# Kernel tuning notes

Measured on AMD Instinct MI355X. Metric: run time of the kernel, lower is better.

The kernel has to match this reference:

```python
import jax, jax.numpy as jnp
import numpy as np

GROUPS = 8
EPS = 1e-5
PERM_IN = {'x': (0, 2, 4, 1, 3), 'y': (0, 2, 3, 1, 4), 'seq': (0, 3, 4, 1, 2)}
PERM_OUT = {'x': (0, 3, 1, 4, 2), 'y': (0, 3, 1, 2, 4), 'seq': (0, 3, 4, 1, 2)}


def bn_train(x, gamma, beta, axis=1):
    """Training-mode batch norm: normalize over all axes except `axis`."""
    axes = tuple(i for i in range(x.ndim) if i != axis)
    mean = x.mean(axes, keepdims=True)
    var = x.var(axes, keepdims=True)
    shp = [1] * x.ndim
    shp[axis] = x.shape[axis]
    return (x - mean) * jax.lax.rsqrt(var + EPS) * gamma.reshape(shp) + beta.reshape(shp)


def axial_attn(x, qkv_w, gq, bq, gs, bs, go, bo, direction):
    # x: (N, C, seq, H, W)
    x = jnp.transpose(x, PERM_IN[direction])
    N, seq, W, C, H = x.shape
    B = N * seq * W
    xf = x.reshape(B, C, H)
    # 1x1 conv1d qkv projection + BN over channels
    qkv = jnp.einsum('oc,bch->boh', qkv_w, xf)            # (B, 2C, H)
    qkv = bn_train(qkv, gq, bq, axis=1)
    gp = C // GROUPS                                       # group_planes
    qkv = qkv.reshape(B, GROUPS, 2 * gp, H)
    q = qkv[:, :, : gp // 2]
    k = qkv[:, :, gp // 2: gp]
    v = qkv[:, :, gp:]
    qk = jnp.einsum('bgci,bgcj->bgij', q, k)               # (B, g, H, H)
    qk = bn_train(qk, gs, bs, axis=1)
    sim = jax.nn.softmax(qk, axis=3)
    sv = jnp.einsum('bgij,bgcj->bgci', sim, v)             # (B, g, gp, H)
    sv = bn_train(sv.reshape(B, C, H), go, bo, axis=1)
    out = sv.reshape(N, seq, W, C, H)
    return jnp.transpose(out, PERM_OUT[direction])


def setup_inputs() -> dict:
    key = jax.random.key(0)
    ks = jax.random.split(key, 4)
    N, C_in, seq, H, W = 2, 128, 16, 56, 56
    width = 64
    x = jax.random.normal(ks[0], (N, C_in, seq, H, W), jnp.float32)
    cd_w = jax.random.normal(ks[1], (width, C_in), jnp.float32) * (1.0 / np.sqrt(C_in))
    qkv_w = jax.random.normal(ks[2], (3, 2 * width, width), jnp.float32) * (1.0 / np.sqrt(width))
    cu_w = jax.random.normal(ks[3], (2 * width, width), jnp.float32) * (1.0 / np.sqrt(width))
    return {
        'x': x,
        'cd_w': cd_w,
        'bn1_g': jnp.ones((width,), jnp.float32),
        'bn1_b': jnp.zeros((width,), jnp.float32),
        'qkv_w': qkv_w,
        'bnq_g': jnp.ones((3, 2 * width), jnp.float32),
        'bnq_b': jnp.zeros((3, 2 * width), jnp.float32),
        'bns_g': jnp.ones((3, GROUPS), jnp.float32),
        'bns_b': jnp.zeros((3, GROUPS), jnp.float32),
        'bno_g': jnp.ones((3, width), jnp.float32),
        'bno_b': jnp.zeros((3, width), jnp.float32),
        'cu_w': cu_w,
        'bn2_g': jnp.ones((2 * width,), jnp.float32),
        'bn2_b': jnp.zeros((2 * width,), jnp.float32),
    }


def reference(x, cd_w, bn1_g, bn1_b, qkv_w, bnq_g, bnq_b, bns_g, bns_b,
              bno_g, bno_b, cu_w, bn2_g, bn2_b):
    identity = x
    out = jnp.einsum('oc,ncshw->noshw', cd_w, x)           # conv_down (1x1)
    out = jax.nn.relu(bn_train(out, bn1_g, bn1_b, axis=1))
    for i, d in enumerate(('x', 'y', 'seq')):              # height, width, seq axial passes
        out = axial_attn(out, qkv_w[i], bnq_g[i], bnq_b[i], bns_g[i], bns_b[i],
                         bno_g[i], bno_b[i], d)
    out = jax.nn.relu(out)
    out = jnp.einsum('oc,ncshw->noshw', cu_w, out)         # conv_up (1x1)
    out = bn_train(out, bn2_g, bn2_b, axis=1)
    return jax.nn.relu(out + identity)
```

## Files before the change

### kernel.cpp

```cpp
#include <hip/hip_runtime.h>

constexpr int SP = 16*56*56;
constexpr int P  = 2*SP;
constexpr float EPSV = 1e-5f;

constexpr size_t SZ_A   = (size_t)2*64*SP;
constexpr size_t OFF_A  = 0;
constexpr size_t OFF_C  = SZ_A;
constexpr size_t OFF_ST = OFF_C + SZ_A;
constexpr size_t OFF_P1 = 0;
constexpr size_t OFF_P2 = 65536;

__global__ void __launch_bounds__(256) kern_down(
    const float* __restrict__ x, const float* __restrict__ w,
    float* __restrict__ A, float* __restrict__ st)
{
  __shared__ float xs[128*64];
  __shared__ float wt[64*129];
  __shared__ float ssum[64], ssq[64];
  const int t = threadIdx.x;
  if (t < 64) { ssum[t] = 0.f; ssq[t] = 0.f; }
  const int p0 = blockIdx.x * 64;
  const int n = p0 / SP, rem = p0 % SP;
  const float* xb = x + (size_t)n*128*SP + rem;
  for (int e4 = t; e4 < 128*16; e4 += 256) {
    int c = e4 >> 4, p4 = (e4 & 15)*4;
    float4 v = *reinterpret_cast<const float4*>(xb + (size_t)c*SP + p4);
    *reinterpret_cast<float4*>(&xs[c*64 + p4]) = v;
  }
  for (int e4 = t; e4 < 64*32; e4 += 256) {
    int o = e4 >> 5, c4 = (e4 & 31)*4;
    float4 v = *reinterpret_cast<const float4*>(w + o*128 + c4);
    *reinterpret_cast<float4*>(&wt[o*129 + c4]) = v;
  }
  __syncthreads();
  const int og = t & 15, pg = t >> 4;
  float acc[4][4] = {};
  for (int c = 0; c < 128; ++c) {
    float xv[4], wv[4];
    #pragma unroll
    for (int j = 0; j < 4; ++j) xv[j] = xs[c*64 + pg*4 + j];
    #pragma unroll
    for (int i = 0; i < 4; ++i) wv[i] = wt[(og + 16*i)*129 + c];
    #pragma unroll
    for (int i = 0; i < 4; ++i) {
      #pragma unroll
      for (int j = 0; j < 4; ++j) acc[i][j] = fmaf(wv[i], xv[j], acc[i][j]);
    }
  }
  float* Ab = A + (size_t)n*64*SP + rem;
  #pragma unroll
  for (int i = 0; i < 4; ++i) {
    const int o = og + 16*i;
    float s1 = 0.f, s2 = 0.f;
    #pragma unroll
    for (int j = 0; j < 4; ++j) { float v = acc[i][j]; s1 += v; s2 += v*v; }
    float4 v4 = make_float4(acc[i][0], acc[i][1], acc[i][2], acc[i][3]);
    *reinterpret_cast<float4*>(Ab + (size_t)o*SP + pg*4) = v4;
    atomicAdd(&ssum[o], s1);
    atomicAdd(&ssq[o], s2);
  }
  __syncthreads();
  if (t < 64) { atomicAdd(&st[t], ssum[t]); atomicAdd(&st[64+t], ssq[t]); }
}

__global__ void __launch_bounds__(256) kern_tr(
    const float* __restrict__ A, float* __restrict__ At)
{
  __shared__ float tile[56*57];
  const size_t base = (size_t)blockIdx.x*3136;
  for (int e4 = threadIdx.x; e4 < 784; e4 += 256) {
    int e = e4*4, h = e/56, w = e%56;
    float4 v = *reinterpret_cast<const float4*>(A + base + e);
    tile[w*57+h] = v.x; tile[(w+1)*57+h] = v.y;
    tile[(w+2)*57+h] = v.z; tile[(w+3)*57+h] = v.w;
  }
  __syncthreads();
  for (int e4 = threadIdx.x; e4 < 784; e4 += 256) {
    int e = e4*4, w = e/56, h = e%56;
    float4 v = make_float4(tile[w*57+h], tile[w*57+h+1], tile[w*57+h+2], tile[w*57+h+3]);
    *reinterpret_cast<float4*>(At + base + e) = v;
  }
}

__global__ void __launch_bounds__(256) kern_up(
    const float* __restrict__ A, const float* __restrict__ w,
    float* __restrict__ U, float* __restrict__ st)
{
  __shared__ float xs[64*64];
  __shared__ float wt[128*65];
  __shared__ float ssum[128], ssq[128];
  const int t = threadIdx.x;
  if (t < 128) { ssum[t]=0.f; ssq[t]=0.f; }
  const int p0 = blockIdx.x*64;
  const int n = p0/SP, rem = p0%SP;
  const float* Ab = A + (size_t)n*64*SP + rem;
  for (int e4 = t; e4 < 64*16; e4 += 256) {
    int c = e4 >> 4, p4 = (e4 & 15)*4;
    float4 v = *reinterpret_cast<const float4*>(Ab + (size_t)c*SP + p4);
    v.x = fmaxf(v.x, 0.f); v.y = fmaxf(v.y, 0.f); v.z = fmaxf(v.z, 0.f); v.w = fmaxf(v.w, 0.f);
    *reinterpret_cast<float4*>(&xs[c*64 + p4]) = v;
  }
  for (int e4 = t; e4 < 128*16; e4 += 256) {
    int o = e4 >> 4, c4 = (e4 & 15)*4;
    float4 v = *reinterpret_cast<const float4*>(w + o*64 + c4);
    *reinterpret_cast<float4*>(&wt[o*65 + c4]) = v;
  }
  __syncthreads();
  const int og = t & 31, pg = t >> 5;
  float acc[4][8] = {};
  for (int c = 0; c < 64; ++c) {
    float xv[8];
    #pragma unroll
    for (int j = 0; j < 8; ++j) xv[j] = xs[c*64 + pg*8 + j];
    #pragma unroll
    for (int i = 0; i < 4; ++i) {
      float wv = wt[(og + 32*i)*65 + c];
      #pragma unroll
      for (int j = 0; j < 8; ++j) acc[i][j] = fmaf(wv, xv[j], acc[i][j]);
    }
  }
  float* Ub = U + (size_t)n*128*SP + rem;
  #pragma unroll
  for (int i = 0; i < 4; ++i) {
    const int o = og + 32*i;
    float s1=0.f, s2=0.f;
    #pragma unroll
    for (int j = 0; j < 8; ++j) { float v = acc[i][j]; s1 += v; s2 += v*v; }
    float4 a = make_float4(acc[i][0],acc[i][1],acc[i][2],acc[i][3]);
    float4 b = make_float4(acc[i][4],acc[i][5],acc[i][6],acc[i][7]);
    *reinterpret_cast<float4*>(Ub + (size_t)o*SP + pg*8)     = a;
    *reinterpret_cast<float4*>(Ub + (size_t)o*SP + pg*8 + 4) = b;
    atomicAdd(&ssum[o], s1); atomicAdd(&ssq[o], s2);
  }
  __syncthreads();
  if (t < 128) { atomicAdd(&st[t], ssum[t]); atomicAdd(&st[128+t], ssq[t]); }
}

template<bool FIRST>
__global__ void __launch_bounds__(256) kern_qkv(
    const float* __restrict__ src, const float* __restrict__ w,
    const float* __restrict__ sc1, const float* __restrict__ sh1,
    float* __restrict__ Bq, float* __restrict__ st)
{
  constexpr int H = 56;
  __shared__ float xs[64*H];
  __shared__ float wt[128*65];
  __shared__ float ssum[128], ssq[128];
  const int t = threadIdx.x;
  if (t < 128) { ssum[t]=0.f; ssq[t]=0.f; }
  const int b = blockIdx.x;
  const int n = b/896, r = b%896, s = r/56, q = r%56;
  const size_t base = (size_t)n*64*SP + s*3136 + q*56;
  for (int e4 = t; e4 < 64*14; e4 += 256) {
    int c = e4/14, j4 = (e4%14)*4;
    float4 v = *reinterpret_cast<const float4*>(src + base + (size_t)c*SP + j4);
    if (FIRST) {
      float sc = sc1[c], sh = sh1[c];
      v.x = fmaxf(fmaf(v.x, sc, sh), 0.f); v.y = fmaxf(fmaf(v.y, sc, sh), 0.f);
      v.z = fmaxf(fmaf(v.z, sc, sh), 0.f); v.w = fmaxf(fmaf(v.w, sc, sh), 0.f);
    }
    xs[c*H + j4]   = v.x; xs[c*H + j4+1] = v.y;
    xs[c*H + j4+2] = v.z; xs[c*H + j4+3] = v.w;
  }
  for (int e4 = t; e4 < 128*16; e4 += 256) {
    int o = e4 >> 4, c4 = (e4 & 15)*4;
    float4 v = *reinterpret_cast<const float4*>(w + o*64 + c4);
    *reinterpret_cast<float4*>(&wt[o*65 + c4]) = v;
  }
  __syncthreads();
  const int og = t & 31, hg = t >> 5;
  float acc[4][7] = {};
  for (int c = 0; c < 64; ++c) {
    float xv[7];
    #pragma unroll
    for (int j = 0; j < 7; ++j) xv[j] = xs[c*H + hg*7 + j];
    #pragma unroll
    for (int i = 0; i < 4; ++i) {
      float wv = wt[(og + 32*i)*65 + c];
      #pragma unroll
      for (int j = 0; j < 7; ++j) acc[i][j] = fmaf(wv, xv[j], acc[i][j]);
    }
  }
  float* ob = Bq + (size_t)b*128*H;
  #pragma unroll
  for (int i = 0; i < 4; ++i) {
    const int o = og + 32*i;
    float s1=0.f, s2=0.f;
    #pragma unroll
    for (int j = 0; j < 7; ++j) {
      float v = acc[i][j];
      ob[o*H + hg*7 + j] = v;
      s1 += v; s2 += v*v;
    }
    atomicAdd(&ssum[o], s1); atomicAdd(&ssq[o], s2);
  }
  __syncthreads();
  if (t < 128) { atomicAdd(&st[t], ssum[t]); atomicAdd(&st[128+t], ssq[t]); }
}

__global__ void __launch_bounds__(256) kern_qkv2(
    const float* __restrict__ A, const float* __restrict__ w,
    float* __restrict__ Bq, float* __restrict__ st)
{
  __shared__ float xs[64*64];
  __shared__ float wt[128*65];
  __shared__ float ssum[128], ssq[128];
  const int t = threadIdx.x;
  if (t < 128) { ssum[t]=0.f; ssq[t]=0.f; }
  const int b = blockIdx.x;
  const int n = b/784, r = b%784, y = r/14, w4 = (r%14)*4;
  const float* Ab = A + (size_t)n*64*SP + y*56 + w4;
  for (int e = t; e < 1024; e += 256) {
    int c = e >> 4, s = e & 15;
    float4 v = *reinterpret_cast<const float4*>(Ab + (size_t)c*SP + s*3136);
    xs[c*64 + s]      = v.x;
    xs[c*64 + 16 + s] = v.y;
    xs[c*64 + 32 + s] = v.z;
    xs[c*64 + 48 + s] = v.w;
  }
  for (int e4 = t; e4 < 128*16; e4 += 256) {
    int o = e4 >> 4, c4 = (e4 & 15)*4;
    float4 v = *reinterpret_cast<const float4*>(w + o*64 + c4);
    *reinterpret_cast<float4*>(&wt[o*65 + c4]) = v;
  }
  __syncthreads();
  const int og = t & 31, cg = t >> 5;
  float acc[4][8] = {};
  for (int c = 0; c < 64; ++c) {
    float xv[8];
    #pragma unroll
    for (int j = 0; j < 8; ++j) xv[j] = xs[c*64 + cg*8 + j];
    #pragma unroll
    for (int i = 0; i < 4; ++i) {
      float wv = wt[(og + 32*i)*65 + c];
      #pragma unroll
      for (int j = 0; j < 8; ++j) acc[i][j] = fmaf(wv, xv[j], acc[i][j]);
    }
  }
  const size_t b0 = (size_t)n*3136 + (size_t)y*56 + w4;
  #pragma unroll
  for (int i = 0; i < 4; ++i) {
    const int o = og + 32*i;
    float s1=0.f, s2=0.f;
    #pragma unroll
    for (int j = 0; j < 8; ++j) {
      int col = cg*8 + j, wl = col >> 4, s = col & 15;
      float v = acc[i][j];
      Bq[(b0 + wl)*2048 + o*16 + s] = v;
      s1 += v; s2 += v*v;
    }
    atomicAdd(&ssum[o], s1); atomicAdd(&ssq[o], s2);
  }
  __syncthreads();
  if (t < 128) { atomicAdd(&st[t], ssum[t]); atomicAdd(&st[128+t], ssq[t]); }
}

__global__ void __launch_bounds__(256) kern_redfin(
    const float* __restrict__ part, const float* __restrict__ g,
    const float* __restrict__ b, float* __restrict__ scsh,
    int nb, int nch, float invc)
{
  const int ch = blockIdx.x;
  const int t = threadIdx.x;
  float s1 = 0.f, s2 = 0.f;
  for (int i = t; i < nb; i += 256) {
    s1 += part[(size_t)i*2*nch + ch];
    s2 += part[(size_t)i*2*nch + nch + ch];
  }
  #pragma unroll
  for (int off = 32; off >= 1; off >>= 1) { s1 += __shfl_xor(s1, off); s2 += __shfl_xor(s2, off); }
  __shared__ float r1[4], r2[4];
  if ((t & 63) == 0) { r1[t>>6] = s1; r2[t>>6] = s2; }
  __syncthreads();
  if (t == 0) {
    float S1 = r1[0]+r1[1]+r1[2]+r1[3], S2 = r2[0]+r2[1]+r2[2]+r2[3];
    float mean = S1*invc, var = S2*invc - mean*mean;
    float sc = g[ch]*rsqrtf(var + EPSV);
    scsh[ch] = sc;
    scsh[nch + ch] = b[ch] - mean*sc;
  }
}

template<int H>
__global__ void __launch_bounds__(256) kern_pass1(
    const float* __restrict__ Bq, const float* __restrict__ qsc,
    const float* __restrict__ qsh, float* __restrict__ part)
{
  constexpr int PW = (H==16) ? 4 : 1;
  const int t = threadIdx.x;
  const int wave = t >> 6, lane = t & 63;
  const int sub = (PW==1) ? 0 : (lane >> 4);
  const int i = (PW==1) ? lane : (lane & 15);
  __shared__ float kls[4][4*H*PW];
  __shared__ float bs[16];
  if (t < 16) bs[t] = 0.f;
  float* klw = kls[wave];
  const int pair0 = (blockIdx.x*4 + wave)*PW;
  for (int e = lane; e < 4*H*PW; e += 64) {
    int sp = e / (4*H), r = e % (4*H);
    int c = r / H, j = r % H;
    int pr = pair0 + sp, bb = pr >> 3, g = pr & 7;
    int o = g*16 + 4 + c;
    klw[e] = fmaf(Bq[((size_t)bb*128 + o)*H + j], qsc[o], qsh[o]);
  }
  __syncthreads();
  const int pr = pair0 + sub, bb = pr >> 3, g = pr & 7;
  const float* kp = klw + sub*4*H;
  const bool act = (i < H);
  float q[4];
  #pragma unroll
  for (int c = 0; c < 4; ++c) {
    int o = g*16 + c;
    q[c] = act ? fmaf(Bq[((size_t)bb*128 + o)*H + i], qsc[o], qsh[o]) : 0.f;
  }
  float s1 = 0.f, s2 = 0.f;
  #pragma unroll
  for (int j = 0; j < H; ++j) {
    float s = q[0]*kp[j] + q[1]*kp[H+j] + q[2]*kp[2*H+j] + q[3]*kp[3*H+j];
    s1 += s; s2 += s*s;
  }
  #pragma unroll
  for (int off = (PW==1?32:8); off >= 1; off >>= 1) {
    s1 += __shfl_xor(s1, off);
    s2 += __shfl_xor(s2, off);
  }
  if ((lane & (PW==1?63:15)) == 0) { atomicAdd(&bs[g], s1); atomicAdd(&bs[8+g], s2); }
  __syncthreads();
  if (t < 16) part[(size_t)blockIdx.x*16 + t] = bs[t];
}

template<int H>
__global__ void __launch_bounds__(256) kern_attn(
    const float* __restrict__ Bq, const float* __restrict__ qsc,
    const float* __restrict__ qsh, const float* __restrict__ ssc,
    float* __restrict__ C, float* __restrict__ part)
{
  constexpr int PW = (H==16) ? 4 : 1;
  const int t = threadIdx.x;
  const int wave = t >> 6, lane = t & 63;
  const int sub = (PW==1) ? 0 : (lane >> 4);
  const int i = (PW==1) ? lane : (lane & 15);
  __shared__ float kv[4][12*H*PW];
  __shared__ float bsum[64], bsq[64];
  if (t < 64) { bsum[t] = 0.f; bsq[t] = 0.f; }
  float* kvw = kv[wave];
  const int pair0 = (blockIdx.x*4 + wave)*PW;
  for (int e = lane; e < 12*H*PW; e += 64) {
    int sp = e / (12*H), r = e % (12*H);
    int c = r / H, j = r % H;
    int pr = pair0 + sp, bb = pr >> 3, g = pr & 7;
    int o = g*16 + 4 + c;
    kvw[e] = fmaf(Bq[((size_t)bb*128 + o)*H + j], qsc[o], qsh[o]);
  }
  __syncthreads();
  const int pr = pair0 + sub, bb = pr >> 3, g = pr & 7;
  const float* kp = kvw + sub*12*H;
  const bool act = (i < H);
  float q[4];
  #pragma unroll
  for (int c = 0; c < 4; ++c) {
    int o = g*16 + c;
    q[c] = act ? fmaf(Bq[((size_t)bb*128 + o)*H + i], qsc[o], qsh[o]) : 0.f;
  }
  const float As = ssc[g];
  float m = -3.4e38f;
  for (int j = 0; j < H; ++j) {
    float s = As * (q[0]*kp[j] + q[1]*kp[H+j] + q[2]*kp[2*H+j] + q[3]*kp[3*H+j]);
    m = fmaxf(m, s);
  }
  float den = 0.f;
  float acc[8] = {};
  for (int j = 0; j < H; ++j) {
    float s = As * (q[0]*kp[j] + q[1]*kp[H+j] + q[2]*kp[2*H+j] + q[3]*kp[3*H+j]);
    float e = __expf(s - m);
    den += e;
    #pragma unroll
    for (int c = 0; c < 8; ++c) acc[c] = fmaf(e, kp[(4+c)*H + j], acc[c]);
  }
  const float inv = 1.f/den;
  #pragma unroll
  for (int c = 0; c < 8; ++c) {
    float vv = act ? acc[c]*inv : 0.f;
    if (act) C[((size_t)bb*64 + g*8 + c)*H + i] = vv;
    float s1 = vv, s2 = vv*vv;
    #pragma unroll
    for (int off = (PW==1?32:8); off >= 1; off >>= 1) {
      s1 += __shfl_xor(s1, off);
      s2 += __shfl_xor(s2, off);
    }
    if ((lane & (PW==1?63:15)) == 0) { atomicAdd(&bsum[g*8+c], s1); atomicAdd(&bsq[g*8+c], s2); }
  }
  __syncthreads();
  if (t < 64) {
    part[(size_t)blockIdx.x*128 + t]      = bsum[t];
    part[(size_t)blockIdx.x*128 + 64 + t] = bsq[t];
  }
}

__global__ void __launch_bounds__(256) kern_scat0(
    const float* __restrict__ C, const float* __restrict__ osc,
    const float* __restrict__ osh, float* __restrict__ A)
{
  __shared__ float tile[56*57];
  const int bid = blockIdx.x;
  const int c = bid & 63, s = (bid >> 6) & 15, n = bid >> 10;
  const float sc = osc[c], sh = osh[c];
  const size_t cb = ((size_t)(n*16+s)*56)*3584 + c*56;
  for (int e = threadIdx.x; e < 3136; e += 256) {
    int w = e/56, h = e%56;
    tile[w*57+h] = C[cb + (size_t)w*3584 + h];
  }
  __syncthreads();
  const size_t ab = ((size_t)(n*64+c)*16+s)*3136;
  for (int e = threadIdx.x; e < 3136; e += 256) {
    int h = e/56, w = e%56;
    A[ab + e] = fmaf(tile[w*57+h], sc, sh);
  }
}

__global__ void __launch_bounds__(256) kern_scat1(
    const float* __restrict__ C, const float* __restrict__ osc,
    const float* __restrict__ osh, float* __restrict__ A)
{
  const int e = blockIdx.x*256 + threadIdx.x;
  if (e >= 1792*64*56) return;
  const int w = e % 56, c = (e/56) & 63, b = e / (56*64);
  const int n = b/896, r = b%896, s = r/56, y = r%56;
  A[((size_t)(n*64+c)*16+s)*3136 + y*56 + w] = fmaf(C[e], osc[c], osh[c]);
}

__global__ void __launch_bounds__(256) kern_scat2(
    const float* __restrict__ C, const float* __restrict__ osc,
    const float* __restrict__ osh, float* __restrict__ A)
{
  __shared__ float tile[56*17];
  const int bid = blockIdx.x;
  const int y = bid % 56, c = (bid/56) & 63, n = bid / 3584;
  const float sc = osc[c], sh = osh[c];
  const size_t cb = ((size_t)(n*56+y)*56)*1024 + c*16;
  for (int e = threadIdx.x; e < 896; e += 256) {
    int w = e >> 4, s = e & 15;
    tile[w*17+s] = C[cb + (size_t)w*1024 + s];
  }
  __syncthreads();
  const size_t ab = (size_t)(n*64+c)*16*3136 + y*56;
  for (int e = threadIdx.x; e < 896; e += 256) {
    int s = e/56, w = e%56;
    A[ab + (size_t)s*3136 + w] = fmaf(tile[w*17+s], sc, sh);
  }
}

__global__ void kern_fin_bn(float* __restrict__ st, const float* __restrict__ g,
                            const float* __restrict__ b, int nch, float invc)
{
  const int t = threadIdx.x;
  if (t < nch) {
    float mean = st[t]*invc;
    float var  = st[nch+t]*invc - mean*mean;
    float sc   = g[t]*rsqrtf(var + EPSV);
    st[2*nch+t] = sc;
    st[3*nch+t] = b[t] - mean*sc;
  }
}

__global__ void __launch_bounds__(256) kern_final(
    float* __restrict__ U, const float* __restrict__ x,
    const float* __restrict__ sc, const float* __restrict__ sh,
    float* __restrict__ out)
{
  const int idx = blockIdx.x*256 + threadIdx.x;
  if (idx >= P*128/4) return;
  const int e = idx*4;
  const int o = (e / SP) & 127;
  float4 u  = *reinterpret_cast<const float4*>(U + e);
  float4 xv = *reinterpret_cast<const float4*>(x + e);
  const float s = sc[o], h = sh[o];
  float4 r;
  r.x = fmaxf(fmaf(u.x, s, h) + xv.x, 0.f);
  r.y = fmaxf(fmaf(u.y, s, h) + xv.y, 0.f);
  r.z = fmaxf(fmaf(u.z, s, h) + xv.z, 0.f);
  r.w = fmaxf(fmaf(u.w, s, h) + xv.w, 0.f);
  *reinterpret_cast<float4*>(out + e) = r;
}

extern "C" void kernel_launch(void* const* d_in, const int* in_sizes, int n_in,
                              void* d_out, int out_size, void* d_ws, size_t ws_size,
                              hipStream_t stream)
{
  const float* x    = (const float*)d_in[0];
  const float* cdw  = (const float*)d_in[1];
  const float* bn1g = (const float*)d_in[2];
  const float* bn1b = (const float*)d_in[3];
  const float* qkvw = (const float*)d_in[4];
  const float* bnqg = (const float*)d_in[5];
  const float* bnqb = (const float*)d_in[6];
  const float* bnsg = (const float*)d_in[7];
  const float* bnsb = (const float*)d_in[8];
  const float* bnog = (const float*)d_in[9];
  const float* bnob = (const float*)d_in[10];
  const float* cuw  = (const float*)d_in[11];
  const float* bn2g = (const float*)d_in[12];
  const float* bn2b = (const float*)d_in[13];
  float* out = (float*)d_out;
  float* ws  = (float*)d_ws;

  float* A   = ws + OFF_A;
  float* C   = ws + OFF_C;
  float* st  = ws + OFF_ST;
  float* Pp1 = ws + OFF_P1;
  float* Pp2 = ws + OFF_P2;
  float* Bq  = out;

  hipMemsetAsync(st, 0, 4096*sizeof(float), stream);

  const float invP = 1.f/100352.f;

  kern_down<<<P/64, 256, 0, stream>>>(x, cdw, A, st);
  kern_fin_bn<<<1, 128, 0, stream>>>(st, bn1g, bn1b, 64, invP);

  {
    float* stq = st + 256; float* sts = stq + 512; float* sto = stq + 544;
    kern_tr<<<2048, 256, 0, stream>>>(A, C);
    kern_qkv<true><<<1792, 256, 0, stream>>>(C, qkvw, st+128, st+192, Bq, stq);
    kern_fin_bn<<<1, 128, 0, stream>>>(stq, bnqg, bnqb, 128, invP);
    kern_pass1<56><<<3584, 256, 0, stream>>>(Bq, stq+256, stq+384, Pp1);
    kern_redfin<<<8, 256, 0, stream>>>(Pp1, bnsg, bnsb, sts, 3584, 8, 1.f/5619712.f);
    kern_attn<56><<<3584, 256, 0, stream>>>(Bq, stq+256, stq+384, sts, C, Pp2);
    kern_redfin<<<64, 256, 0, stream>>>(Pp2, bnog, bnob, sto, 3584, 64, invP);
    kern_scat0<<<2048, 256, 0, stream>>>(C, sto, sto+64, A);
  }
  {
    float* stq = st + 256 + 1024; float* sts = stq + 512; float* sto = stq + 544;
    kern_qkv<false><<<1792, 256, 0, stream>>>(A, qkvw+8192, st, st, Bq, stq);
    kern_fin_bn<<<1, 128, 0, stream>>>(stq, bnqg+128, bnqb+128, 128, invP);
    kern_pass1<56><<<3584, 256, 0, stream>>>(Bq, stq+256, stq+384, Pp1);
    kern_redfin<<<8, 256, 0, stream>>>(Pp1, bnsg+8, bnsb+8, sts, 3584, 8, 1.f/5619712.f);
    kern_attn<56><<<3584, 256, 0, stream>>>(Bq, stq+256, stq+384, sts, C, Pp2);
    kern_redfin<<<64, 256, 0, stream>>>(Pp2, bnog+64, bnob+64, sto, 3584, 64, invP);
    kern_scat1<<<25088, 256, 0, stream>>>(C, sto, sto+64, A);
  }
  {
    float* stq = st + 256 + 2048; float* sts = stq + 512; float* sto = stq + 544;
    kern_qkv2<<<1568, 256, 0, stream>>>(A, qkvw+16384, Bq, stq);
    kern_fin_bn<<<1, 128, 0, stream>>>(stq, bnqg+256, bnqb+256, 128, invP);
    kern_pass1<16><<<3136, 256, 0, stream>>>(Bq, stq+256, stq+384, Pp1);
    kern_redfin<<<8, 256, 0, stream>>>(Pp1, bnsg+16, bnsb+16, sts, 3136, 8, 1.f/1605632.f);
    kern_attn<16><<<3136, 256, 0, stream>>>(Bq, stq+256, stq+384, sts, C, Pp2);
    kern_redfin<<<64, 256, 0, stream>>>(Pp2, bnog+128, bnob+128, sto, 3136, 64, invP);
    kern_scat2<<<7168, 256, 0, stream>>>(C, sto, sto+64, A);
  }

  float* st2 = st + 3328;
  kern_up<<<P/64, 256, 0, stream>>>(A, cuw, Bq, st2);
  kern_fin_bn<<<1, 128, 0, stream>>>(st2, bn2g, bn2b, 128, invP);
  kern_final<<<P*128/4/256, 256, 0, stream>>>(Bq, x, st2+256, st2+384, out);
}
```

Measured before the change: 661.1 us.

## Fold BN finalize into consumer kernels, vectorize scat1, pre-transpose for seq qkv

Removes the five single-block kern_fin_bn launches. Each consumer kernel (qkv, pass1, attn, final) now computes the BN scale and shift from the raw sums into shared memory, trading a little redundant per-block math for fewer serialized launches. kern_scat1 now handles four elements per thread with float4 loads and stores, replacing scalar scattered stores. A new kern_tr2 transposes A into a seq-innermost layout so kern_qkv2 can use contiguous float4 loads instead of strided gathers, at the cost of an extra full-tensor read and write.

```diff
diff --git a/kernel.cpp b/kernel.cpp
--- a/kernel.cpp
+++ b/kernel.cpp
@@ -3,6 +3,7 @@
 constexpr int SP = 16*56*56;
 constexpr int P  = 2*SP;
 constexpr float EPSV = 1e-5f;
+constexpr float INVP = 1.f/100352.f;
 
 constexpr size_t SZ_A   = (size_t)2*64*SP;
 constexpr size_t OFF_A  = 0;
@@ -80,6 +81,31 @@
     int e = e4*4, w = e/56, h = e%56;
     float4 v = make_float4(tile[w*57+h], tile[w*57+h+1], tile[w*57+h+2], tile[w*57+h+3]);
     *reinterpret_cast<float4*>(At + base + e) = v;
+  }
+}
+
+__global__ void __launch_bounds__(256) kern_tr2(
+    const float* __restrict__ A, float* __restrict__ At2)
+{
+  __shared__ float tile[16*785];
+  const int bid = blockIdx.x;
+  const int slice = bid >> 2, hw0 = (bid & 3)*784;
+  const float* Asrc = A + (size_t)slice*SP + hw0;
+  for (int e4 = threadIdx.x; e4 < 3136; e4 += 256) {
+    int s = e4/196, h4 = (e4%196)*4;
+    float4 v = *reinterpret_cast<const float4*>(Asrc + (size_t)s*3136 + h4);
+    tile[s*785 + h4]   = v.x; tile[s*785 + h4+1] = v.y;
+    tile[s*785 + h4+2] = v.z; tile[s*785 + h4+3] = v.w;
+  }
+  __syncthreads();
+  float* dst = At2 + ((size_t)slice*3136 + hw0)*16;
+  for (int hw = threadIdx.x; hw < 784; hw += 256) {
+    #pragma unroll
+    for (int sq = 0; sq < 4; ++sq) {
+      float4 v = make_float4(tile[(4*sq)*785 + hw], tile[(4*sq+1)*785 + hw],
+                             tile[(4*sq+2)*785 + hw], tile[(4*sq+3)*785 + hw]);
+      *reinterpret_cast<float4*>(dst + (size_t)hw*16 + sq*4) = v;
+    }
   }
 }
 
@@ -140,15 +166,26 @@
 template<bool FIRST>
 __global__ void __launch_bounds__(256) kern_qkv(
     const float* __restrict__ src, const float* __restrict__ w,
-    const float* __restrict__ sc1, const float* __restrict__ sh1,
+    const float* __restrict__ st1, const float* __restrict__ g1,
+    const float* __restrict__ b1,
     float* __restrict__ Bq, float* __restrict__ st)
 {
   constexpr int H = 56;
   __shared__ float xs[64*H];
   __shared__ float wt[128*65];
   __shared__ float ssum[128], ssq[128];
+  __shared__ float sc1s[64], sh1s[64];
   const int t = threadIdx.x;
   if (t < 128) { ssum[t]=0.f; ssq[t]=0.f; }
+  if (FIRST) {
+    if (t < 64) {
+      float mean = st1[t]*INVP;
+      float var  = st1[64+t]*INVP - mean*mean;
+      float sc   = g1[t]*rsqrtf(var + EPSV);
+      sc1s[t] = sc; sh1s[t] = b1[t] - mean*sc;
+    }
+    __syncthreads();
+  }
   const int b = blockIdx.x;
   const int n = b/896, r = b%896, s = r/56, q = r%56;
   const size_t base = (size_t)n*64*SP + s*3136 + q*56;
@@ -156,7 +193,7 @@
     int c = e4/14, j4 = (e4%14)*4;
     float4 v = *reinterpret_cast<const float4*>(src + base + (size_t)c*SP + j4);
     if (FIRST) {
-      float sc = sc1[c], sh = sh1[c];
+      float sc = sc1s[c], sh = sh1s[c];
       v.x = fmaxf(fmaf(v.x, sc, sh), 0.f); v.y = fmaxf(fmaf(v.y, sc, sh), 0.f);
       v.z = fmaxf(fmaf(v.z, sc, sh), 0.f); v.w = fmaxf(fmaf(v.w, sc, sh), 0.f);
     }
@@ -200,7 +237,7 @@
 }
 
 __global__ void __launch_bounds__(256) kern_qkv2(
-    const float* __restrict__ A, const float* __restrict__ w,
+    const float* __restrict__ At2, const float* __restrict__ w,
     float* __restrict__ Bq, float* __restrict__ st)
 {
   __shared__ float xs[64*64];
@@ -210,14 +247,11 @@
   if (t < 128) { ssum[t]=0.f; ssq[t]=0.f; }
   const int b = blockIdx.x;
   const int n = b/784, r = b%784, y = r/14, w4 = (r%14)*4;
-  const float* Ab = A + (size_t)n*64*SP + y*56 + w4;
-  for (int e = t; e < 1024; e += 256) {
-    int c = e >> 4, s = e & 15;
-    float4 v = *reinterpret_cast<const float4*>(Ab + (size_t)c*SP + s*3136);
-    xs[c*64 + s]      = v.x;
-    xs[c*64 + 16 + s] = v.y;
-    xs[c*64 + 32 + s] = v.z;
-    xs[c*64 + 48 + s] = v.w;
+  for (int e4 = t; e4 < 1024; e4 += 256) {
+    int c = e4 >> 4, rr = e4 & 15, wl = rr >> 2, s4 = (rr & 3)*4;
+    float4 v = *reinterpret_cast<const float4*>(
+        At2 + (((size_t)(n*64+c)*3136) + y*56 + w4 + wl)*16 + s4);
+    *reinterpret_cast<float4*>(&xs[c*64 + wl*16 + s4]) = v;
   }
   for (int e4 = t; e4 < 128*16; e4 += 256) {
     int o = e4 >> 4, c4 = (e4 & 15)*4;
@@ -284,8 +318,9 @@
 
 template<int H>
 __global__ void __launch_bounds__(256) kern_pass1(
-    const float* __restrict__ Bq, const float* __restrict__ qsc,
-    const float* __restrict__ qsh, float* __restrict__ part)
+    const float* __restrict__ Bq, const float* __restrict__ stq,
+    const float* __restrict__ gq, const float* __restrict__ bq,
+    float* __restrict__ part)
 {
   constexpr int PW = (H==16) ? 4 : 1;
   const int t = threadIdx.x;
@@ -294,7 +329,15 @@
   const int i = (PW==1) ? lane : (lane & 15);
   __shared__ float kls[4][4*H*PW];
   __shared__ float bs[16];
+  __shared__ float qscs[128], qshs[128];
   if (t < 16) bs[t] = 0.f;
+  if (t < 128) {
+    float mean = stq[t]*INVP;
+    float var  = stq[128+t]*INVP - mean*mean;
+    float sc   = gq[t]*rsqrtf(var + EPSV);
+    qscs[t] = sc; qshs[t] = bq[t] - mean*sc;
+  }
+  __syncthreads();
   float* klw = kls[wave];
   const int pair0 = (blockIdx.x*4 + wave)*PW;
   for (int e = lane; e < 4*H*PW; e += 64) {
@@ -302,7 +345,7 @@
     int c = r / H, j = r % H;
     int pr = pair0 + sp, bb = pr >> 3, g = pr & 7;
     int o = g*16 + 4 + c;
-    klw[e] = fmaf(Bq[((size_t)bb*128 + o)*H + j], qsc[o], qsh[o]);
+    klw[e] = fmaf(Bq[((size_t)bb*128 + o)*H + j], qscs[o], qshs[o]);
   }
   __syncthreads();
   const int pr = pair0 + sub, bb = pr >> 3, g = pr & 7;
@@ -312,7 +355,7 @@
   #pragma unroll
   for (int c = 0; c < 4; ++c) {
     int o = g*16 + c;
-    q[c] = act ? fmaf(Bq[((size_t)bb*128 + o)*H + i], qsc[o], qsh[o]) : 0.f;
+    q[c] = act ? fmaf(Bq[((size_t)bb*128 + o)*H + i], qscs[o], qshs[o]) : 0.f;
   }
   float s1 = 0.f, s2 = 0.f;
   #pragma unroll
@@ -332,8 +375,9 @@
 
 template<int H>
 __global__ void __launch_bounds__(256) kern_attn(
-    const float* __restrict__ Bq, const float* __restrict__ qsc,
-    const float* __restrict__ qsh, const float* __restrict__ ssc,
+    const float* __restrict__ Bq, const float* __restrict__ stq,
+    const float* __restrict__ gq, const float* __restrict__ bq,
+    const float* __restrict__ ssc,
     float* __restrict__ C, float* __restrict__ part)
 {
   constexpr int PW = (H==16) ? 4 : 1;
@@ -343,7 +387,15 @@
   const int i = (PW==1) ? lane : (lane & 15);
   __shared__ float kv[4][12*H*PW];
   __shared__ float bsum[64], bsq[64];
+  __shared__ float qscs[128], qshs[128];
   if (t < 64) { bsum[t] = 0.f; bsq[t] = 0.f; }
+  if (t < 128) {
+    float mean = stq[t]*INVP;
+    float var  = stq[128+t]*INVP - mean*mean;
+    float sc   = gq[t]*rsqrtf(var + EPSV);
+    qscs[t] = sc; qshs[t] = bq[t] - mean*sc;
+  }
+  __syncthreads();
   float* kvw = kv[wave];
   const int pair0 = (blockIdx.x*4 + wave)*PW;
   for (int e = lane; e < 12*H*PW; e += 64) {
@@ -351,7 +403,7 @@
     int c = r / H, j = r % H;
     int pr = pair0 + sp, bb = pr >> 3, g = pr & 7;
     int o = g*16 + 4 + c;
-    kvw[e] = fmaf(Bq[((size_t)bb*128 + o)*H + j], qsc[o], qsh[o]);
+    kvw[e] = fmaf(Bq[((size_t)bb*128 + o)*H + j], qscs[o], qshs[o]);
   }
   __syncthreads();
   const int pr = pair0 + sub, bb = pr >> 3, g = pr & 7;
@@ -361,7 +413,7 @@
   #pragma unroll
   for (int c = 0; c < 4; ++c) {
     int o = g*16 + c;
-    q[c] = act ? fmaf(Bq[((size_t)bb*128 + o)*H + i], qsc[o], qsh[o]) : 0.f;
+    q[c] = act ? fmaf(Bq[((size_t)bb*128 + o)*H + i], qscs[o], qshs[o]) : 0.f;
   }
   const float As = ssc[g];
   float m = -3.4e38f;
@@ -423,11 +475,15 @@
     const float* __restrict__ C, const float* __restrict__ osc,
     const float* __restrict__ osh, float* __restrict__ A)
 {
-  const int e = blockIdx.x*256 + threadIdx.x;
-  if (e >= 1792*64*56) return;
-  const int w = e % 56, c = (e/56) & 63, b = e / (56*64);
+  const int e4 = blockIdx.x*256 + threadIdx.x;
+  if (e4 >= 1792*64*14) return;
+  const int w4 = (e4 % 14)*4, c = (e4/14) & 63, b = e4 / (14*64);
   const int n = b/896, r = b%896, s = r/56, y = r%56;
-  A[((size_t)(n*64+c)*16+s)*3136 + y*56 + w] = fmaf(C[e], osc[c], osh[c]);
+  const float sc = osc[c], sh = osh[c];
+  float4 v = *reinterpret_cast<const float4*>(C + ((size_t)b*64 + c)*56 + w4);
+  v.x = fmaf(v.x, sc, sh); v.y = fmaf(v.y, sc, sh);
+  v.z = fmaf(v.z, sc, sh); v.w = fmaf(v.w, sc, sh);
+  *reinterpret_cast<float4*>(A + ((size_t)(n*64+c)*16+s)*3136 + y*56 + w4) = v;
 }
 
 __global__ void __launch_bounds__(256) kern_scat2(
@@ -451,31 +507,27 @@
   }
 }
 
-__global__ void kern_fin_bn(float* __restrict__ st, const float* __restrict__ g,
-                            const float* __restrict__ b, int nch, float invc)
-{
-  const int t = threadIdx.x;
-  if (t < nch) {
-    float mean = st[t]*invc;
-    float var  = st[nch+t]*invc - mean*mean;
-    float sc   = g[t]*rsqrtf(var + EPSV);
-    st[2*nch+t] = sc;
-    st[3*nch+t] = b[t] - mean*sc;
-  }
-}
-
 __global__ void __launch_bounds__(256) kern_final(
     float* __restrict__ U, const float* __restrict__ x,
-    const float* __restrict__ sc, const float* __restrict__ sh,
-    float* __restrict__ out)
-{
-  const int idx = blockIdx.x*256 + threadIdx.x;
+    const float* __restrict__ st2, const float* __restrict__ g2,
+    const float* __restrict__ b2, float* __restrict__ out)
+{
+  __shared__ float scs[128], shs[128];
+  const int t = threadIdx.x;
+  if (t < 128) {
+    float mean = st2[t]*INVP;
+    float var  = st2[128+t]*INVP - mean*mean;
+    float sc   = g2[t]*rsqrtf(var + EPSV);
+    scs[t] = sc; shs[t] = b2[t] - mean*sc;
+  }
+  __syncthreads();
+  const int idx = blockIdx.x*256 + t;
   if (idx >= P*128/4) return;
   const int e = idx*4;
   const int o = (e / SP) & 127;
   float4 u  = *reinterpret_cast<const float4*>(U + e);
   float4 xv = *reinterpret_cast<const float4*>(x + e);
-  const float s = sc[o], h = sh[o];
+  const float s = scs[o], h = shs[o];
   float4 r;
   r.x = fmaxf(fmaf(u.x, s, h) + xv.x, 0.f);
   r.y = fmaxf(fmaf(u.y, s, h) + xv.y, 0.f);
@@ -514,45 +566,39 @@
 
   hipMemsetAsync(st, 0, 4096*sizeof(float), stream);
 
-  const float invP = 1.f/100352.f;
-
   kern_down<<<P/64, 256, 0, stream>>>(x, cdw, A, st);
-  kern_fin_bn<<<1, 128, 0, stream>>>(st, bn1g, bn1b, 64, invP);
 
   {
     float* stq = st + 256; float* sts = stq + 512; float* sto = stq + 544;
     kern_tr<<<2048, 256, 0, stream>>>(A, C);
-    kern_qkv<true><<<1792, 256, 0, stream>>>(C, qkvw, st+128, st+192, Bq, stq);
-    kern_fin_bn<<<1, 128, 0, stream>>>(stq, bnqg, bnqb, 128, invP);
-    kern_pass1<56><<<3584, 256, 0, stream>>>(Bq, stq+256, stq+384, Pp1);
+    kern_qkv<true><<<1792, 256, 0, stream>>>(C, qkvw, st, bn1g, bn1b, Bq, stq);
+    kern_pass1<56><<<3584, 256, 0, stream>>>(Bq, stq, bnqg, bnqb, Pp1);
     kern_redfin<<<8, 256, 0, stream>>>(Pp1, bnsg, bnsb, sts, 3584, 8, 1.f/5619712.f);
-    kern_attn<56><<<3584, 256, 0, stream>>>(Bq, stq+256, stq+384, sts, C, Pp2);
-    kern_redfin<<<64, 256, 0, stream>>>(Pp2, bnog, bnob, sto, 3584, 64, invP);
+    kern_attn<56><<<3584, 256, 0, stream>>>(Bq, stq, bnqg, bnqb, sts, C, Pp2);
+    kern_redfin<<<64, 256, 0, stream>>>(Pp2, bnog, bnob, sto, 3584, 64, INVP);
     kern_scat0<<<2048, 256, 0, stream>>>(C, sto, sto+64, A);
   }
   {
     float* stq = st + 256 + 1024; float* sts = stq + 512; float* sto = stq + 544;
-    kern_qkv<false><<<1792, 256, 0, stream>>>(A, qkvw+8192, st, st, Bq, stq);
-    kern_fin_bn<<<1, 128, 0, stream>>>(stq, bnqg+128, bnqb+128, 128, invP);
-    kern_pass1<56><<<3584, 256, 0, stream>>>(Bq, stq+256, stq+384, Pp1);
+    kern_qkv<false><<<1792, 256, 0, stream>>>(A, qkvw+8192, st, bn1g, bn1b, Bq, stq);
+    kern_pass1<56><<<3584, 256, 0, stream>>>(Bq, stq, bnqg+128, bnqb+128, Pp1);
     kern_redfin<<<8, 256, 0, stream>>>(Pp1, bnsg+8, bnsb+8, sts, 3584, 8, 1.f/5619712.f);
-    kern_attn<56><<<3584, 256, 0, stream>>>(Bq, stq+256, stq+384, sts, C, Pp2);
-    kern_redfin<<<64, 256, 0, stream>>>(Pp2, bnog+64, bnob+64, sto, 3584, 64, invP);
-    kern_scat1<<<25088, 256, 0, stream>>>(C, sto, sto+64, A);
+    kern_attn<56><<<3584, 256, 0, stream>>>(Bq, stq, bnqg+128, bnqb+128, sts, C, Pp2);
+    kern_redfin<<<64, 256, 0, stream>>>(Pp2, bnog+64, bnob+64, sto, 3584, 64, INVP);
+    kern_scat1<<<6272, 256, 0, stream>>>(C, sto, sto+64, A);
   }
   {
     float* stq = st + 256 + 2048; float* sts = stq + 512; float* sto = stq + 544;
-    kern_qkv2<<<1568, 256, 0, stream>>>(A, qkvw+16384, Bq, stq);
-    kern_fin_bn<<<1, 128, 0, stream>>>(stq, bnqg+256, bnqb+256, 128, invP);
-    kern_pass1<16><<<3136, 256, 0, stream>>>(Bq, stq+256, stq+384, Pp1);
+    kern_tr2<<<512, 256, 0, stream>>>(A, C);
+    kern_qkv2<<<1568, 256, 0, stream>>>(C, qkvw+16384, Bq, stq);
+    kern_pass1<16><<<3136, 256, 0, stream>>>(Bq, stq, bnqg+256, bnqb+256, Pp1);
     kern_redfin<<<8, 256, 0, stream>>>(Pp1, bnsg+16, bnsb+16, sts, 3136, 8, 1.f/1605632.f);
-    kern_attn<16><<<3136, 256, 0, stream>>>(Bq, stq+256, stq+384, sts, C, Pp2);
-    kern_redfin<<<64, 256, 0, stream>>>(Pp2, bnog+128, bnob+128, sto, 3136, 64, invP);
+    kern_attn<16><<<3136, 256, 0, stream>>>(Bq, stq, bnqg+256, bnqb+256, sts, C, Pp2);
+    kern_redfin<<<64, 256, 0, stream>>>(Pp2, bnog+128, bnob+128, sto, 3136, 64, INVP);
     kern_scat2<<<7168, 256, 0, stream>>>(C, sto, sto+64, A);
   }
 
   float* st2 = st + 3328;
   kern_up<<<P/64, 256, 0, stream>>>(A, cuw, Bq, st2);
-  kern_fin_bn<<<1, 128, 0, stream>>>(st2, bn2g, bn2b, 128, invP);
-  kern_final<<<P*128/4/256, 256, 0, stream>>>(Bq, x, st2+256, st2+384, out);
-}
+  kern_final<<<P*128/4/256, 256, 0, stream>>>(Bq, x, st2, bn2g, bn2b, out);
+}
```

Result: no change. 651.1 us (-1.5%).
